# Performance work log

Hardware: AMD Instinct MI355X
Metric: run time of the kernel (lower is better)

Reference implementation:

```python
import jax, jax.numpy as jnp
import numpy as np

B, T, C, H = 4, 2048, 1024, 16
HD = C // H
INIT_SCALE = 0.25

def setup_inputs() -> dict:
    key = jax.random.key(0)
    k1, k2, k3 = jax.random.split(key, 3)
    x = jax.random.normal(k1, (B, T, C), dtype=jnp.float32)
    W_attn = jax.random.normal(k2, (3 * C, C), dtype=jnp.float32) * INIT_SCALE  # torch Linear weight [out,in]
    b_attn = jnp.zeros((3 * C,), dtype=jnp.float32)
    W_proj = jax.random.normal(k3, (C, C), dtype=jnp.float32) * INIT_SCALE
    b_proj = jnp.zeros((C,), dtype=jnp.float32)
    return {"x": x, "W_attn": W_attn, "b_attn": b_attn, "W_proj": W_proj, "b_proj": b_proj}

def reference(x, W_attn, b_attn, W_proj, b_proj):
    # fused QKV projection: [B,T,3C]
    qkv = x @ W_attn.T + b_attn
    q, k, v = jnp.split(qkv, 3, axis=-1)  # each [B,T,C]
    # [B,H,T,HD]
    q = q.reshape(B, T, H, HD).transpose(0, 2, 1, 3)
    k = k.reshape(B, T, H, HD).transpose(0, 2, 1, 3)
    v = v.reshape(B, T, H, HD).transpose(0, 2, 1, 3)
    scale = 1.0 / jnp.sqrt(jnp.asarray(HD, dtype=q.dtype))
    attn = jnp.einsum('bhqd,bhkd->bhqk', q, k) * scale  # [B,H,T,T]
    attn = jax.nn.softmax(attn, axis=-1)
    out = jnp.einsum('bhqk,bhkd->bhqd', attn, v)  # [B,H,T,HD]
    out = out.transpose(0, 2, 1, 3).reshape(B, T, C)
    return out @ W_proj.T + b_proj
```

## Files before the change

### kernel.cpp

```cpp
#include <hip/hip_runtime.h>
#include <hip/hip_bf16.h>

#define BB 4
#define TT 2048
#define CC 1024
#define HH 16
#define HD 64

typedef _Float16 half8 __attribute__((ext_vector_type(8)));
typedef _Float16 half4 __attribute__((ext_vector_type(4)));
typedef _Float16 half2_t __attribute__((ext_vector_type(2)));
typedef __fp16 fp16x2 __attribute__((ext_vector_type(2)));
typedef float floatx4 __attribute__((ext_vector_type(4)));
typedef float floatx16 __attribute__((ext_vector_type(16)));
typedef int intx2 __attribute__((ext_vector_type(2)));
typedef int intx4 __attribute__((ext_vector_type(4)));

__device__ __forceinline__ void async_cp16(const void* g, void* l) {
    __builtin_amdgcn_global_load_lds(
        (const __attribute__((address_space(1))) unsigned int*)g,
        (__attribute__((address_space(3))) unsigned int*)l,
        16, 0, 0);
}

__device__ __forceinline__ float exp2_raw(float x) {
    return __builtin_amdgcn_exp2f(x);
}

__device__ __forceinline__ int pkh(float a, float b) {
    fp16x2 v = __builtin_amdgcn_cvt_pkrtz(a, b);
    return __builtin_bit_cast(int, v);
}

__device__ __forceinline__ float maxv16(floatx16 s) {
    float a0 = fmaxf(fmaxf(s[0], s[1]), s[2]);
    float a1 = fmaxf(fmaxf(s[3], s[4]), s[5]);
    float a2 = fmaxf(fmaxf(s[6], s[7]), s[8]);
    float a3 = fmaxf(fmaxf(s[9], s[10]), s[11]);
    float a4 = fmaxf(fmaxf(s[12], s[13]), s[14]);
    float b0 = fmaxf(fmaxf(a0, a1), a2);
    float b1 = fmaxf(fmaxf(a3, a4), s[15]);
    return fmaxf(b0, b1);
}

__device__ __forceinline__ half8 assembleF(int a, int b, int c, int d) {
    intx2 s1 = __builtin_amdgcn_permlane32_swap(a, c, false, false);
    intx2 s2 = __builtin_amdgcn_permlane32_swap(b, d, false, false);
    intx4 w = {s1[0], s2[0], s1[1], s2[1]};
    return __builtin_bit_cast(half8, w);
}

__global__ void cvt_f32_f16(const float* __restrict__ src, _Float16* __restrict__ dst, int n) {
    int i = (blockIdx.x * blockDim.x + threadIdx.x) * 8;
    if (i < n) {
        float4 v0 = *(const float4*)(src + i);
        float4 v1 = *(const float4*)(src + i + 4);
        half8 h;
        h[0] = (_Float16)v0.x; h[1] = (_Float16)v0.y; h[2] = (_Float16)v0.z; h[3] = (_Float16)v0.w;
        h[4] = (_Float16)v1.x; h[5] = (_Float16)v1.y; h[6] = (_Float16)v1.z; h[7] = (_Float16)v1.w;
        *(half8*)(dst + i) = h;
    }
}

template <int EPI>
__global__ __launch_bounds__(256) void hgemm_nt(
    const _Float16* __restrict__ A, const _Float16* __restrict__ Bw,
    const float* __restrict__ bias,
    _Float16* __restrict__ q_out, _Float16* __restrict__ k_out, _Float16* __restrict__ v_out,
    float* __restrict__ c_out,
    int M, int N, int K)
{
    __shared__ __attribute__((aligned(16))) _Float16 As[2 * 128 * 32];
    __shared__ __attribute__((aligned(16))) _Float16 Bs[2 * 128 * 32];

    const int tid  = threadIdx.x;
    const int lane = tid & 63;
    const int wave = tid >> 6;
    const int quad = lane >> 4;
    const int lc   = lane & 15;
    const int wr   = wave >> 1, wc = wave & 1;
    const size_t bm = (size_t)blockIdx.y * 128;
    const size_t bn = (size_t)blockIdx.x * 128;

    const int r0 = tid >> 2;
    const int ck = (tid & 3) * 8;

    const _Float16* Ap = A + (bm + r0) * (size_t)K + ck;
    const _Float16* Bp = Bw + (bn + r0) * (size_t)K + ck;
    _Float16* lA = As + tid * 8;
    _Float16* lB = Bs + tid * 8;
    const size_t rstep = (size_t)64 * K;

    floatx4 acc[4][4] = {};

    for (int kk = 0; kk < K; kk += 64) {
        __syncthreads();
        async_cp16(Ap + kk, lA);
        async_cp16(Ap + kk + rstep, lA + 2048);
        async_cp16(Ap + kk + 32, lA + 4096);
        async_cp16(Ap + kk + 32 + rstep, lA + 4096 + 2048);
        async_cp16(Bp + kk, lB);
        async_cp16(Bp + kk + rstep, lB + 2048);
        async_cp16(Bp + kk + 32, lB + 4096);
        async_cp16(Bp + kk + 32 + rstep, lB + 4096 + 2048);
        __syncthreads();

#pragma unroll
        for (int h = 0; h < 2; h++) {
            half8 af[4], bf[4];
#pragma unroll
            for (int mt = 0; mt < 4; mt++)
                af[mt] = *(const half8*)(As + h * 4096 + (wr * 64 + mt * 16 + lc) * 32 + quad * 8);
#pragma unroll
            for (int nt = 0; nt < 4; nt++)
                bf[nt] = *(const half8*)(Bs + h * 4096 + (wc * 64 + nt * 16 + lc) * 32 + quad * 8);
#pragma unroll
            for (int mt = 0; mt < 4; mt++)
#pragma unroll
                for (int nt = 0; nt < 4; nt++)
                    acc[mt][nt] = __builtin_amdgcn_mfma_f32_16x16x32_f16(af[mt], bf[nt], acc[mt][nt], 0, 0, 0);
        }
    }

#pragma unroll
    for (int mt = 0; mt < 4; mt++) {
        int mbase = (int)bm + wr * 64 + mt * 16 + quad * 4;
#pragma unroll
        for (int nt = 0; nt < 4; nt++) {
            int n = (int)bn + wc * 64 + nt * 16 + lc;
            float bv = bias[n];
#pragma unroll
            for (int r = 0; r < 4; r++) {
                float v = acc[mt][nt][r] + bv;
                int mm = mbase + r;
                if (EPI == 0) {
                    int seg = n >> 10;
                    int cm  = n & 1023;
                    int h = cm >> 6, d = cm & 63;
                    int bb = mm >> 11, t = mm & 2047;
                    size_t dst = (((size_t)(bb * HH + h)) * TT + t) * HD + d;
                    if (seg == 0)      q_out[dst] = (_Float16)(v * 0.18033688f);
                    else if (seg == 1) k_out[dst] = (_Float16)v;
                    else               v_out[dst] = (_Float16)v;
                } else {
                    c_out[(size_t)mm * N + n] = v;
                }
            }
        }
    }
}

__global__ __launch_bounds__(512) void attn_flash(
    const _Float16* __restrict__ Qp, const _Float16* __restrict__ Kp,
    const _Float16* __restrict__ Vp, _Float16* __restrict__ Op)
{
    __shared__ __attribute__((aligned(16))) _Float16 Ks[64 * 64];
    __shared__ __attribute__((aligned(16))) _Float16 Vt[64 * 64];

    const int bh   = blockIdx.x;
    const int qt   = blockIdx.y;
    const int tid  = threadIdx.x;
    const int lane = tid & 63;
    const int wave = tid >> 6;
    const int ql   = lane & 31;
    const int hi   = lane >> 5;

    const size_t hb = (size_t)bh * TT * HD;

    const int qrow = qt * 256 + wave * 32 + ql;
    half8 bq[4];
#pragma unroll
    for (int c = 0; c < 4; c++)
        bq[c] = *(const half8*)(Qp + hb + (size_t)qrow * HD + c * 16 + hi * 8);

    floatx16 o0 = (floatx16)0.0f, o1 = (floatx16)0.0f;
    float mrun = -1e30f, lrun = 0.f;

    const int sk = tid >> 3;
    const int sj = tid & 7;
    const int sg = sj ^ (sk & 7);
    const _Float16* Kg = Kp + hb + (size_t)sk * HD + sg * 8;
    _Float16* KsW = Ks + tid * 8;

    const int vkp = tid >> 4;
    const int vd4 = (tid & 15) * 4;
    const _Float16* Vg0 = Vp + hb + (size_t)(2 * vkp) * HD + vd4;
    const _Float16* Vg1 = Vg0 + HD;

    half8 kv  = *(const half8*)Kg;
    half4 va0 = *(const half4*)Vg0;
    half4 vb0 = *(const half4*)Vg1;

    for (int kt = 0; kt < TT; kt += 64) {
        __syncthreads();
        *(half8*)KsW = kv;
#pragma unroll
        for (int j = 0; j < 4; j++) {
            int row = vd4 + j;
            int boff = (row * 128 + vkp * 4) ^ (((row >> 2) & 7) << 4);
            half2_t w; w[0] = va0[j]; w[1] = vb0[j];
            *(half2_t*)((char*)Vt + boff) = w;
        }
        __syncthreads();

        if (kt + 64 < TT) {
            const size_t koff = (size_t)(kt + 64) * HD;
            kv  = *(const half8*)(Kg + koff);
            va0 = *(const half4*)(Vg0 + koff);
            vb0 = *(const half4*)(Vg1 + koff);
        }

        floatx16 s0 = (floatx16)0.0f, s1 = (floatx16)0.0f;
        __builtin_amdgcn_s_setprio(1);
#pragma unroll
        for (int c = 0; c < 4; c++) {
            int offk = (ql * 128 + c * 32 + hi * 16) ^ ((ql & 7) << 4);
            half8 a0 = *(const half8*)((const char*)Ks + offk);
            half8 a1 = *(const half8*)((const char*)Ks + offk + 4096);
            s0 = __builtin_amdgcn_mfma_f32_32x32x16_f16(a0, bq[c], s0, 0, 0, 0);
            s1 = __builtin_amdgcn_mfma_f32_32x32x16_f16(a1, bq[c], s1, 0, 0, 0);
        }
        __builtin_amdgcn_s_setprio(0);

        float mx = fmaxf(maxv16(s0), maxv16(s1));
        mx = fmaxf(mx, __shfl_xor(mx, 32));
        const bool noresc = __all(mx <= mrun + 8.0f);
        const float mnew = noresc ? mrun : fmaxf(mrun, mx);
        float rs = 0.f;
        int d[16];
#pragma unroll
        for (int i = 0; i < 8; i++) {
            float e0 = exp2_raw(s0[2 * i] - mnew);
            float e1 = exp2_raw(s0[2 * i + 1] - mnew);
            rs += e0 + e1;
            d[i] = pkh(e0, e1);
        }
#pragma unroll
        for (int i = 0; i < 8; i++) {
            float e0 = exp2_raw(s1[2 * i] - mnew);
            float e1 = exp2_raw(s1[2 * i + 1] - mnew);
            rs += e0 + e1;
            d[8 + i] = pkh(e0, e1);
        }
        rs += __shfl_xor(rs, 32);
        if (!noresc) {
            float al = exp2_raw(mrun - mnew);
            mrun = mnew;
            lrun *= al;
            o0 *= al;
            o1 *= al;
        }
        lrun += rs;

        half8 F[4];
        F[0] = assembleF(d[0], d[1], d[2], d[3]);
        F[1] = assembleF(d[4], d[5], d[6], d[7]);
        F[2] = assembleF(d[8], d[9], d[10], d[11]);
        F[3] = assembleF(d[12], d[13], d[14], d[15]);

        __builtin_amdgcn_s_setprio(1);
#pragma unroll
        for (int kb = 0; kb < 4; kb++) {
            int offv = (ql * 128 + kb * 32 + hi * 16) ^ (((ql >> 2) & 7) << 4);
            half8 v0 = *(const half8*)((const char*)Vt + offv);
            half8 v1 = *(const half8*)((const char*)Vt + offv + 4096);
            o0 = __builtin_amdgcn_mfma_f32_32x32x16_f16(v0, F[kb], o0, 0, 0, 0);
            o1 = __builtin_amdgcn_mfma_f32_32x32x16_f16(v1, F[kb], o1, 0, 0, 0);
        }
        __builtin_amdgcn_s_setprio(0);
    }

    const float inv = __builtin_amdgcn_rcpf(lrun);
    const int b = bh >> 4, h = bh & 15;
    size_t base = ((size_t)(b * TT + qrow)) * CC + h * HD;
#pragma unroll
    for (int rr = 0; rr < 4; rr++) {
        half4 hv0, hv1;
#pragma unroll
        for (int t = 0; t < 4; t++) {
            hv0[t] = (_Float16)(o0[rr * 4 + t] * inv);
            hv1[t] = (_Float16)(o1[rr * 4 + t] * inv);
        }
        *(half4*)(Op + base + 8 * rr + 4 * hi) = hv0;
        *(half4*)(Op + base + 32 + 8 * rr + 4 * hi) = hv1;
    }
}

extern "C" void kernel_launch(void* const* d_in, const int* in_sizes, int n_in,
                              void* d_out, int out_size, void* d_ws, size_t ws_size,
                              hipStream_t stream) {
    const float* x      = (const float*)d_in[0];
    const float* W_attn = (const float*)d_in[1];
    const float* b_attn = (const float*)d_in[2];
    const float* W_proj = (const float*)d_in[3];
    const float* b_proj = (const float*)d_in[4];
    float* out = (float*)d_out;

    const size_t SZ_XH  = (size_t)BB * TT * CC * 2;
    const size_t SZ_WA  = (size_t)3 * CC * CC * 2;
    const size_t SZ_WP  = (size_t)CC * CC * 2;
    const size_t SZ_QKV = (size_t)BB * HH * TT * HD * 2;
    size_t off = 0;
    _Float16* xh  = (_Float16*)((char*)d_ws + off); off += SZ_XH;
    _Float16* wah = (_Float16*)((char*)d_ws + off); off += SZ_WA;
    _Float16* wph = (_Float16*)((char*)d_ws + off); off += SZ_WP;
    _Float16* Qh  = (_Float16*)((char*)d_ws + off); off += SZ_QKV;
    _Float16* Kh  = (_Float16*)((char*)d_ws + off); off += SZ_QKV;
    _Float16* Vh  = (_Float16*)((char*)d_ws + off); off += SZ_QKV;
    _Float16* Ah  = (_Float16*)((char*)d_ws + off); off += SZ_XH;
    if (ws_size < off) return;

    const int NX  = BB * TT * CC;
    const int NWA = 3 * CC * CC;
    const int NWP = CC * CC;
    cvt_f32_f16<<<NX / 8 / 256, 256, 0, stream>>>(x, xh, NX);
    cvt_f32_f16<<<NWA / 8 / 256, 256, 0, stream>>>(W_attn, wah, NWA);
    cvt_f32_f16<<<NWP / 8 / 256, 256, 0, stream>>>(W_proj, wph, NWP);

    hgemm_nt<0><<<dim3(3 * CC / 128, BB * TT / 128), 256, 0, stream>>>(
        xh, wah, b_attn, Qh, Kh, Vh, nullptr, BB * TT, 3 * CC, CC);

    attn_flash<<<dim3(BB * HH, TT / 256), 512, 0, stream>>>(Qh, Kh, Vh, Ah);

    hgemm_nt<1><<<dim3(CC / 128, BB * TT / 128), 256, 0, stream>>>(
        Ah, wph, b_proj, nullptr, nullptr, nullptr, out, BB * TT, CC, CC);
}
```

Before: 276.2 us.

## Use 256x256 tiled QKV GEMM with XOR-swizzled LDS and 64-wide K steps

Replaces the templated 128x128 QKV GEMM with a dedicated 512-thread kernel that computes 256x256 output tiles using a K-step of 64, double-buffered async global-to-LDS copies, an XOR swizzle on LDS columns to avoid bank conflicts, and s_setprio around the MFMA bursts. The larger tile is meant to raise arithmetic intensity and cut global and LDS traffic per FLOP for the largest GEMM. The grid shrinks to 12x32 blocks, which may leave the 256 CUs underfilled or unevenly loaded. The 128 KB of LDS per block plus heavy accumulator register use also limit occupancy. The projection GEMM is split out as its own non-templated kernel with unchanged behaviour.

```diff
diff --git a/kernel.cpp b/kernel.cpp
--- a/kernel.cpp
+++ b/kernel.cpp
@@ -62,12 +62,126 @@
     }
 }
 
-template <int EPI>
-__global__ __launch_bounds__(256) void hgemm_nt(
+__global__ __launch_bounds__(512, 2) void hgemm256_qkv(
     const _Float16* __restrict__ A, const _Float16* __restrict__ Bw,
     const float* __restrict__ bias,
     _Float16* __restrict__ q_out, _Float16* __restrict__ k_out, _Float16* __restrict__ v_out,
-    float* __restrict__ c_out,
+    int M, int N, int K)
+{
+    __shared__ __attribute__((aligned(16))) _Float16 LA[2 * 256 * 64];
+    __shared__ __attribute__((aligned(16))) _Float16 LB[2 * 256 * 64];
+
+    const int tid  = threadIdx.x;
+    const int lane = tid & 63;
+    const int wave = tid >> 6;
+    const int quad = lane >> 4;
+    const int lc   = lane & 15;
+    const int wr   = wave >> 2;
+    const int wn   = wave & 3;
+    const size_t bm = (size_t)blockIdx.y * 256;
+    const size_t bn = (size_t)blockIdx.x * 256;
+
+    const int srow  = tid >> 3;
+    const int sphys = (tid & 7) ^ (srow & 7);
+    const _Float16* Asrc = A + (bm + srow) * (size_t)K + sphys * 8;
+    const _Float16* Bsrc = Bw + (bn + srow) * (size_t)K + sphys * 8;
+    const size_t rquad = (size_t)64 * K;
+
+    const int xr = lc & 7;
+
+    floatx4 acc[8][4] = {};
+
+#define STAGE256(bufi, kk) do {                                         \
+        _Float16* da = LA + (bufi) * 16384 + tid * 8;                   \
+        _Float16* db = LB + (bufi) * 16384 + tid * 8;                   \
+        const _Float16* sa = Asrc + (kk);                               \
+        const _Float16* sb = Bsrc + (kk);                               \
+        async_cp16(sa,             da);                                 \
+        async_cp16(sa + rquad,     da + 4096);                          \
+        async_cp16(sa + 2 * rquad, da + 8192);                          \
+        async_cp16(sa + 3 * rquad, da + 12288);                         \
+        async_cp16(sb,             db);                                 \
+        async_cp16(sb + rquad,     db + 4096);                          \
+        async_cp16(sb + 2 * rquad, db + 8192);                          \
+        async_cp16(sb + 3 * rquad, db + 12288);                         \
+    } while (0)
+
+    STAGE256(0, 0);
+    STAGE256(1, 64);
+
+    const int NTT = K / 64;
+    for (int t = 0; t < NTT; ++t) {
+        if (t < NTT - 2) asm volatile("s_waitcnt vmcnt(8)" ::: "memory");
+        else             asm volatile("s_waitcnt vmcnt(0)" ::: "memory");
+        __builtin_amdgcn_s_barrier();
+        __builtin_amdgcn_sched_barrier(0);
+
+        const _Float16* Abuf = LA + (t & 1) * 16384;
+        const _Float16* Bbuf = LB + (t & 1) * 16384;
+
+        half8 bf[4][2];
+#pragma unroll
+        for (int nt = 0; nt < 4; nt++) {
+            int row = wn * 64 + nt * 16 + lc;
+#pragma unroll
+            for (int kh = 0; kh < 2; kh++)
+                bf[nt][kh] = *(const half8*)(Bbuf + row * 64 + ((kh * 4 + quad) ^ xr) * 8);
+        }
+#pragma unroll
+        for (int mh = 0; mh < 2; mh++) {
+            half8 af[4][2];
+#pragma unroll
+            for (int mt = 0; mt < 4; mt++) {
+                int row = wr * 128 + mh * 64 + mt * 16 + lc;
+#pragma unroll
+                for (int kh = 0; kh < 2; kh++)
+                    af[mt][kh] = *(const half8*)(Abuf + row * 64 + ((kh * 4 + quad) ^ xr) * 8);
+            }
+            __builtin_amdgcn_s_setprio(1);
+#pragma unroll
+            for (int mt = 0; mt < 4; mt++)
+#pragma unroll
+                for (int nt = 0; nt < 4; nt++) {
+                    acc[mh * 4 + mt][nt] = __builtin_amdgcn_mfma_f32_16x16x32_f16(
+                        af[mt][0], bf[nt][0], acc[mh * 4 + mt][nt], 0, 0, 0);
+                    acc[mh * 4 + mt][nt] = __builtin_amdgcn_mfma_f32_16x16x32_f16(
+                        af[mt][1], bf[nt][1], acc[mh * 4 + mt][nt], 0, 0, 0);
+                }
+            __builtin_amdgcn_s_setprio(0);
+        }
+        __builtin_amdgcn_s_barrier();
+        __builtin_amdgcn_sched_barrier(0);
+        if (t + 2 < NTT) STAGE256(t & 1, (t + 2) * 64);
+    }
+#undef STAGE256
+
+#pragma unroll
+    for (int MT = 0; MT < 8; MT++) {
+        int mbase = (int)bm + wr * 128 + MT * 16 + quad * 4;
+#pragma unroll
+        for (int nt = 0; nt < 4; nt++) {
+            int n = (int)bn + wn * 64 + nt * 16 + lc;
+            float bv = bias[n];
+#pragma unroll
+            for (int r = 0; r < 4; r++) {
+                float v = acc[MT][nt][r] + bv;
+                int mm = mbase + r;
+                int seg = n >> 10;
+                int cm  = n & 1023;
+                int h = cm >> 6, d = cm & 63;
+                int bb = mm >> 11, tt = mm & 2047;
+                size_t dst = (((size_t)(bb * HH + h)) * TT + tt) * HD + d;
+                if (seg == 0)      q_out[dst] = (_Float16)(v * 0.18033688f);
+                else if (seg == 1) k_out[dst] = (_Float16)v;
+                else               v_out[dst] = (_Float16)v;
+            }
+        }
+    }
+}
+
+__global__ __launch_bounds__(256) void hgemm_nt_proj(
+    const _Float16* __restrict__ A, const _Float16* __restrict__ Bw,
+    const float* __restrict__ bias, float* __restrict__ c_out,
     int M, int N, int K)
 {
     __shared__ __attribute__((aligned(16))) _Float16 As[2 * 128 * 32];
@@ -130,22 +244,8 @@
             int n = (int)bn + wc * 64 + nt * 16 + lc;
             float bv = bias[n];
 #pragma unroll
-            for (int r = 0; r < 4; r++) {
-                float v = acc[mt][nt][r] + bv;
-                int mm = mbase + r;
-                if (EPI == 0) {
-                    int seg = n >> 10;
-                    int cm  = n & 1023;
-                    int h = cm >> 6, d = cm & 63;
-                    int bb = mm >> 11, t = mm & 2047;
-                    size_t dst = (((size_t)(bb * HH + h)) * TT + t) * HD + d;
-                    if (seg == 0)      q_out[dst] = (_Float16)(v * 0.18033688f);
-                    else if (seg == 1) k_out[dst] = (_Float16)v;
-                    else               v_out[dst] = (_Float16)v;
-                } else {
-                    c_out[(size_t)mm * N + n] = v;
-                }
-            }
+            for (int r = 0; r < 4; r++)
+                c_out[(size_t)(mbase + r) * N + n] = acc[mt][nt][r] + bv;
         }
     }
 }
@@ -317,11 +417,11 @@
     cvt_f32_f16<<<NWA / 8 / 256, 256, 0, stream>>>(W_attn, wah, NWA);
     cvt_f32_f16<<<NWP / 8 / 256, 256, 0, stream>>>(W_proj, wph, NWP);
 
-    hgemm_nt<0><<<dim3(3 * CC / 128, BB * TT / 128), 256, 0, stream>>>(
-        xh, wah, b_attn, Qh, Kh, Vh, nullptr, BB * TT, 3 * CC, CC);
+    hgemm256_qkv<<<dim3(3 * CC / 256, BB * TT / 256), 512, 0, stream>>>(
+        xh, wah, b_attn, Qh, Kh, Vh, BB * TT, 3 * CC, CC);
 
     attn_flash<<<dim3(BB * HH, TT / 256), 512, 0, stream>>>(Qh, Kh, Vh, Ah);
 
-    hgemm_nt<1><<<dim3(CC / 128, BB * TT / 128), 256, 0, stream>>>(
-        Ah, wph, b_proj, nullptr, nullptr, nullptr, out, BB * TT, CC, CC);
-}
+    hgemm_nt_proj<<<dim3(CC / 128, BB * TT / 128), 256, 0, stream>>>(
+        Ah, wph, b_proj, out, BB * TT, CC, CC);
+}
```

After: 276.8 us. About the same (+0.2%).
